# Kernel optimization log

Hardware: AMD Instinct MI355X
Metric: run time of the kernel (lower is better)

Reference implementation:

```python
import jax, jax.numpy as jnp
from jax import lax
import numpy as np

MB, QLEN, EMB, QVS, VOCAB, ANS = 64, 20, 32, 128, 80, 10
CH, D, NOBJ, OBJF, G = 24, 8, 64, 26, 256


def _coord_tensor():
    c = np.zeros((NOBJ, 2), dtype=np.float32)
    for i in range(NOBJ):
        c[i] = [(i // 8 - 2) / 2.0, (i % 8 - 2) / 2.0]
    return jnp.asarray(c)


def conv_bn_relu(x, w, b, g, beta):
    y = lax.conv_general_dilated(x, w, (2, 2), [(1, 1), (1, 1)],
                                 dimension_numbers=("NCHW", "OIHW", "NCHW"))
    y = y + b[None, :, None, None]
    m = y.mean((0, 2, 3), keepdims=True)
    v = y.var((0, 2, 3), keepdims=True)  # biased var, training-mode BN
    y = (y - m) / jnp.sqrt(v + 1e-5) * g[None, :, None, None] + beta[None, :, None, None]
    return jax.nn.relu(y)


def lstm_last(xseq, wih, whh, bih, bhh):
    # xseq: [T, mb, E]; PyTorch gate order i,f,g,o
    H = whh.shape[1]
    h0 = jnp.zeros((xseq.shape[1], H), xseq.dtype)

    def step(carry, x_t):
        h, c = carry
        gates = x_t @ wih.T + bih + h @ whh.T + bhh
        i, f, g, o = jnp.split(gates, 4, axis=-1)
        c = jax.nn.sigmoid(f) * c + jax.nn.sigmoid(i) * jnp.tanh(g)
        h = jax.nn.sigmoid(o) * jnp.tanh(c)
        return (h, c), None

    (h, _), _ = lax.scan(step, (h0, h0), xseq)
    return h


def setup_inputs() -> dict:
    key = jax.random.key(0)
    ks = iter(jax.random.split(key, 64))
    nrm = lambda shape, s=0.05: jax.random.normal(next(ks), shape, jnp.float32) * s
    d = {}
    d["image"] = jax.random.normal(next(ks), (MB, 3, 128, 128), jnp.float32)
    d["question"] = jax.random.randint(next(ks), (MB, QLEN), 0, VOCAB, jnp.int32)
    emb = nrm((VOCAB, EMB), 1.0)
    d["emb"] = emb.at[0].set(0.0)  # padding_idx=0
    d["lstm_wih"] = nrm((4 * QVS, EMB))
    d["lstm_whh"] = nrm((4 * QVS, QVS))
    d["lstm_bih"] = nrm((4 * QVS,))
    d["lstm_bhh"] = nrm((4 * QVS,))
    cin = 3
    for l in range(1, 5):
        d[f"c{l}_w"] = nrm((CH, cin, 3, 3))
        d[f"c{l}_b"] = nrm((CH,))
        d[f"bn{l}_g"] = jnp.ones((CH,), jnp.float32)
        d[f"bn{l}_b"] = jnp.zeros((CH,), jnp.float32)
        cin = CH
    d["g1_w"] = nrm((G, 2 * OBJF + QVS))
    d["g1_b"] = nrm((G,))
    for l in (2, 3, 4):
        d[f"g{l}_w"] = nrm((G, G))
        d[f"g{l}_b"] = nrm((G,))
    d["f1_w"] = nrm((G, G)); d["f1_b"] = nrm((G,))
    d["f2_w"] = nrm((G, G)); d["f2_b"] = nrm((G,))
    d["f3_w"] = nrm((ANS, G)); d["f3_b"] = nrm((ANS,))
    return d


def reference(image, question, emb, lstm_wih, lstm_whh, lstm_bih, lstm_bhh,
              c1_w, c1_b, bn1_g, bn1_b, c2_w, c2_b, bn2_g, bn2_b,
              c3_w, c3_b, bn3_g, bn3_b, c4_w, c4_b, bn4_g, bn4_b,
              g1_w, g1_b, g2_w, g2_b, g3_w, g3_b, g4_w, g4_b,
              f1_w, f1_b, f2_w, f2_b, f3_w, f3_b):
    # question -> LSTM final hidden state
    q = emb[question]                      # [mb, T, E]
    q = jnp.transpose(q, (1, 0, 2))        # [T, mb, E]
    qvec = lstm_last(q, lstm_wih, lstm_whh, lstm_bih, lstm_bhh)  # [mb, QVS]

    # conv tower: 128 -> 64 -> 32 -> 16 -> 8
    x = conv_bn_relu(image, c1_w, c1_b, bn1_g, bn1_b)
    x = conv_bn_relu(x, c2_w, c2_b, bn2_g, bn2_b)
    x = conv_bn_relu(x, c3_w, c3_b, bn3_g, bn3_b)
    x = conv_bn_relu(x, c4_w, c4_b, bn4_g, bn4_b)  # [mb, 24, 8, 8]

    # objects = flattened grid cells + coords -> [mb, 64, 26]
    x_flat = x.reshape(MB, CH, NOBJ).transpose(0, 2, 1)
    coords = jnp.broadcast_to(_coord_tensor()[None], (MB, NOBJ, 2))
    objs = jnp.concatenate([x_flat, coords], axis=-1)

    # g_theta fc1 decomposed over the concat [obj_c(26), obj_r(26), q(128)]
    # so the 180-wide pairwise tensor is never materialized.
    w_i, w_j, w_q = g1_w[:, :OBJF], g1_w[:, OBJF:2 * OBJF], g1_w[:, 2 * OBJF:]
    pre_i = objs @ w_i.T                   # contribution of x_i (column object)
    pre_j = objs @ w_j.T                   # contribution of x_j (row object)
    pre_q = qvec @ w_q.T + g1_b            # [mb, 256]
    h = jax.nn.relu(pre_j[:, :, None, :] + pre_i[:, None, :, :]
                    + pre_q[:, None, None, :])      # [mb, 64, 64, 256]
    h = jax.nn.relu(h @ g2_w.T + g2_b)
    h = jax.nn.relu(h @ g3_w.T + g3_b)
    h = jax.nn.relu(h @ g4_w.T + g4_b)
    x_g = h.sum((1, 2))                    # sum over all 4096 pairs -> [mb, 256]

    # f_phi (dropout as identity / eval mode)
    x_f = jax.nn.relu(x_g @ f1_w.T + f1_b)
    x_f = jax.nn.relu(x_f @ f2_w.T + f2_b)
    x_f = x_f @ f3_w.T + f3_b
    return jax.nn.log_softmax(x_f, axis=-1)
```

## Files before the change

kernel.cpp:

```cpp
#include <hip/hip_runtime.h>
#include <math.h>

#define MBS   64
#define QLENS 20
#define EMBS  32
#define QVSS  128
#define ANSS  10
#define CHS   24
#define NOBJS 64
#define GS    256

typedef __attribute__((ext_vector_type(8))) short short8;
typedef __attribute__((ext_vector_type(4))) float f32x4;
typedef __attribute__((ext_vector_type(16))) float f32x16;

__device__ __forceinline__ unsigned short f2bf(float f) {
  unsigned u = __float_as_uint(f);
  u += 0x7fffu + ((u >> 16) & 1u);
  return (unsigned short)(u >> 16);
}
__device__ __forceinline__ float sigm(float x) { return 1.0f / (1.0f + expf(-x)); }

__global__ __launch_bounds__(256) void prep_k(const float* __restrict__ g2w,
                                              const float* __restrict__ g3w,
                                              const float* __restrict__ g4w,
                                              unsigned short* __restrict__ wbf,
                                              const float* __restrict__ g1w,
                                              float* __restrict__ g1wT,
                                              float* __restrict__ stats) {
  int bidx = blockIdx.x;
  if (bidx == 0) stats[threadIdx.x] = 0.0f;
  if (bidx < 768) {
    int idx = bidx * 256 + threadIdx.x;
    int l = idx >> 16, r = idx & 65535;
    int kt = r >> 12;
    int rem = r & 4095;
    int kh = rem >> 11;
    int n = (rem >> 3) & 255;
    int e = rem & 7;
    const float* src = (l == 0) ? g2w : ((l == 1) ? g3w : g4w);
    wbf[idx] = f2bf(src[n * 256 + kt * 16 + kh * 8 + e]);
  } else {
    int idx = (bidx - 768) * 256 + threadIdx.x;
    int f = idx >> 8, n = idx & 255;
    g1wT[f * 256 + n] = g1w[n * 180 + f];
  }
}

__global__ __launch_bounds__(512) void lstm_k(const int* __restrict__ question,
                                              const float* __restrict__ emb,
                                              const float* __restrict__ wih,
                                              const float* __restrict__ bih,
                                              const float* __restrict__ bhh,
                                              const float* __restrict__ whh,
                                              float* __restrict__ qvec) {
  int b = blockIdx.x;
  int gt = threadIdx.x;
  __shared__ float h[QVSS];
  __shared__ float gates[4 * QVSS];
  __shared__ int toks[QLENS];
  float w[QVSS];
#pragma unroll
  for (int k = 0; k < QVSS; ++k) w[k] = whh[gt * QVSS + k];
  float wi[EMBS];
#pragma unroll
  for (int k = 0; k < EMBS; ++k) wi[k] = wih[gt * EMBS + k];
  float bb = bih[gt] + bhh[gt];
  if (gt < QLENS) toks[gt] = question[b * QLENS + gt];
  float c = 0.0f;
  if (gt < QVSS) h[gt] = 0.0f;
  __syncthreads();
  float xp[QLENS];
#pragma unroll
  for (int t = 0; t < QLENS; ++t) {
    const float* e = emb + toks[t] * EMBS;
    float a = bb;
#pragma unroll
    for (int k = 0; k < EMBS; ++k) a += wi[k] * e[k];
    xp[t] = a;
  }
  for (int t = 0; t < QLENS; ++t) {
    float acc = xp[t];
#pragma unroll
    for (int k4 = 0; k4 < QVSS / 4; ++k4) {
      float4 hv = *reinterpret_cast<const float4*>(&h[k4 * 4]);
      acc += w[k4 * 4 + 0] * hv.x + w[k4 * 4 + 1] * hv.y
           + w[k4 * 4 + 2] * hv.z + w[k4 * 4 + 3] * hv.w;
    }
    gates[gt] = acc;
    __syncthreads();
    if (gt < QVSS) {
      float ig = gates[gt];
      float fg = gates[QVSS + gt];
      float gg = gates[2 * QVSS + gt];
      float og = gates[3 * QVSS + gt];
      c = sigm(fg) * c + sigm(ig) * tanhf(gg);
      h[gt] = sigm(og) * tanhf(c);
    }
    __syncthreads();
  }
  if (gt < QVSS) qvec[b * QVSS + gt] = h[gt];
}

template <int CIN, int H, bool BN>
__global__ __launch_bounds__(256) void conv_k(const float* __restrict__ x,
                                              const float* __restrict__ w,
                                              const float* __restrict__ bias,
                                              float* __restrict__ y,
                                              const float* __restrict__ st,
                                              const float* __restrict__ g,
                                              const float* __restrict__ beta,
                                              float inv_cnt) {
  const int OH = H / 2, GW = OH / 4, CP = CHS / 2;
  __shared__ float4 swp[CHS * CIN * 3];
  __shared__ float sb[CHS];
  __shared__ float ss[CIN], stt[CIN];
  for (int i = threadIdx.x; i < CHS * CIN * 3; i += 256) {
    int kh = i % 3, ci = (i / 3) % CIN, co = i / (3 * CIN);
    const float* wp = w + (co * CIN + ci) * 9 + kh * 3;
    swp[i] = make_float4(wp[0], wp[1], wp[2], 0.0f);
  }
  if (threadIdx.x < CHS) sb[threadIdx.x] = bias[threadIdx.x];
  if (BN && threadIdx.x < CIN) {
    int ci = threadIdx.x;
    float m = st[ci * 2 + 0] * inv_cnt;
    float v = st[ci * 2 + 1] * inv_cnt - m * m;
    float r = rsqrtf(v + 1e-5f);
    ss[ci] = r * g[ci];
    stt[ci] = beta[ci] - m * r * g[ci];
  }
  __syncthreads();
  int idx = blockIdx.x * 256 + threadIdx.x;
  int gg = idx % GW;
  int oh = (idx / GW) % OH;
  int cp = (idx / (GW * OH)) % CP;
  int b  = idx / (CP * OH * GW);
  int co0 = cp * 2, co1 = co0 + 1;
  float a00 = sb[co0], a01 = a00, a02 = a00, a03 = a00;
  float a10 = sb[co1], a11 = a10, a12 = a10, a13 = a10;
  const float* xb = x + b * CIN * H * H;
  const float4* w0 = swp + co0 * CIN * 3;
  const float4* w1 = swp + co1 * CIN * 3;
  bool left = (gg > 0);
#pragma unroll
  for (int kh = 0; kh < 3; ++kh) {
    int ih = oh * 2 - 1 + kh;
    if (ih < 0 || ih >= H) continue;
    for (int ci = 0; ci < CIN; ++ci) {
      const float* row = xb + (ci * H + ih) * H + 8 * gg;
      float4 v1 = *(const float4*)(row);
      float4 v2 = *(const float4*)(row + 4);
      float am1 = left ? row[-1] : 0.0f;
      if (BN) {
        float s = ss[ci], t = stt[ci];
        v1.x = fmaxf(fmaf(v1.x, s, t), 0.0f);
        v1.y = fmaxf(fmaf(v1.y, s, t), 0.0f);
        v1.z = fmaxf(fmaf(v1.z, s, t), 0.0f);
        v1.w = fmaxf(fmaf(v1.w, s, t), 0.0f);
        v2.x = fmaxf(fmaf(v2.x, s, t), 0.0f);
        v2.y = fmaxf(fmaf(v2.y, s, t), 0.0f);
        v2.z = fmaxf(fmaf(v2.z, s, t), 0.0f);
        v2.w = fmaxf(fmaf(v2.w, s, t), 0.0f);
        am1 = left ? fmaxf(fmaf(am1, s, t), 0.0f) : 0.0f;
      }
      float4 wa = w0[ci * 3 + kh];
      float4 wb = w1[ci * 3 + kh];
      a00 = fmaf(wa.x, am1,  a00); a00 = fmaf(wa.y, v1.x, a00); a00 = fmaf(wa.z, v1.y, a00);
      a01 = fmaf(wa.x, v1.y, a01); a01 = fmaf(wa.y, v1.z, a01); a01 = fmaf(wa.z, v1.w, a01);
      a02 = fmaf(wa.x, v1.w, a02); a02 = fmaf(wa.y, v2.x, a02); a02 = fmaf(wa.z, v2.y, a02);
      a03 = fmaf(wa.x, v2.y, a03); a03 = fmaf(wa.y, v2.z, a03); a03 = fmaf(wa.z, v2.w, a03);
      a10 = fmaf(wb.x, am1,  a10); a10 = fmaf(wb.y, v1.x, a10); a10 = fmaf(wb.z, v1.y, a10);
      a11 = fmaf(wb.x, v1.y, a11); a11 = fmaf(wb.y, v1.z, a11); a11 = fmaf(wb.z, v1.w, a11);
      a12 = fmaf(wb.x, v1.w, a12); a12 = fmaf(wb.y, v2.x, a12); a12 = fmaf(wb.z, v2.y, a12);
      a13 = fmaf(wb.x, v2.y, a13); a13 = fmaf(wb.y, v2.z, a13); a13 = fmaf(wb.z, v2.w, a13);
    }
  }
  *(float4*)(y + ((b * CHS + co0) * OH + oh) * OH + 4 * gg) = make_float4(a00, a01, a02, a03);
  *(float4*)(y + ((b * CHS + co1) * OH + oh) * OH + 4 * gg) = make_float4(a10, a11, a12, a13);
}

__global__ __launch_bounds__(256) void stats_k(const float* __restrict__ y,
                                               float* __restrict__ st,
                                               int HW, int SUB) {
  int c = blockIdx.x / SUB, sub = blockIdx.x % SUB;
  int bpb = MBS / SUB;
  float s = 0.0f, s2 = 0.0f;
  for (int b = sub * bpb; b < (sub + 1) * bpb; ++b) {
    const float* p = y + (b * CHS + c) * HW;
    for (int i = threadIdx.x * 4; i < HW; i += 1024) {
      float4 v = *reinterpret_cast<const float4*>(p + i);
      s  += v.x + v.y + v.z + v.w;
      s2 += v.x * v.x + v.y * v.y + v.z * v.z + v.w * v.w;
    }
  }
#pragma unroll
  for (int off = 1; off < 64; off <<= 1) {
    s  += __shfl_xor(s, off);
    s2 += __shfl_xor(s2, off);
  }
  __shared__ float rs[4], rs2[4];
  int w = threadIdx.x >> 6;
  if ((threadIdx.x & 63) == 0) { rs[w] = s; rs2[w] = s2; }
  __syncthreads();
  if (threadIdx.x == 0) {
    atomicAdd(&st[c * 2 + 0], rs[0] + rs[1] + rs[2] + rs[3]);
    atomicAdd(&st[c * 2 + 1], rs2[0] + rs2[1] + rs2[2] + rs2[3]);
  }
}

__global__ __launch_bounds__(256) void pre_k(const float* __restrict__ x4raw,
                                             const float* __restrict__ st,
                                             const float* __restrict__ g,
                                             const float* __restrict__ beta,
                                             const float* __restrict__ g1wT,
                                             const float* __restrict__ g1b,
                                             const float* __restrict__ qvec,
                                             float* __restrict__ pre_i,
                                             float* __restrict__ pre_j,
                                             float* __restrict__ pre_q) {
  int bo = blockIdx.x;
  int n = threadIdx.x;
  __shared__ float sm[QVSS];
  if (bo < 4096) {
    int b = bo >> 6, o = bo & 63;
    if (n < CHS) {
      float m = st[n * 2 + 0] * (1.0f / 4096.0f);
      float v = st[n * 2 + 1] * (1.0f / 4096.0f) - m * m;
      float xv = x4raw[(b * CHS + n) * NOBJS + o];
      sm[n] = fmaxf((xv - m) * rsqrtf(v + 1e-5f) * g[n] + beta[n], 0.0f);
    }
    if (n == 24) sm[24] = (float)(o / 8 - 2) * 0.5f;
    if (n == 25) sm[25] = (float)(o % 8 - 2) * 0.5f;
    __syncthreads();
    float ai = 0.0f, aj = 0.0f;
#pragma unroll
    for (int f = 0; f < 26; ++f) {
      ai += g1wT[f * 256 + n] * sm[f];
      aj += g1wT[(26 + f) * 256 + n] * sm[f];
    }
    pre_i[bo * GS + n] = ai;
    pre_j[bo * GS + n] = aj;
  } else {
    int b = bo - 4096;
    if (n < QVSS) sm[n] = qvec[b * QVSS + n];
    __syncthreads();
    float a = g1b[n];
#pragma unroll
    for (int k = 0; k < QVSS; ++k) a += g1wT[(52 + k) * 256 + n] * sm[k];
    pre_q[b * GS + n] = a;
  }
}

__global__ __launch_bounds__(512, 4) void rel_k(const float* __restrict__ pre_i,
                                                const float* __restrict__ pre_j,
                                                const float* __restrict__ pre_q,
                                                const unsigned short* __restrict__ wbf,
                                                const float* __restrict__ g2b,
                                                const float* __restrict__ g3b,
                                                const float* __restrict__ g4b,
                                                float* __restrict__ xpart) {
  __shared__ short8 hb8[2048];
  char* hb = (char*)hb8;
  int bid = blockIdx.x;
  int b = bid >> 6, j = bid & 63;
  int tid = threadIdx.x;
  int w = tid >> 6, lane = tid & 63;
  int l31 = lane & 31, lh = lane >> 5;

  const short8* Wt = (const short8*)wbf;
  const int nA = w * 32 + l31;
  const int pOff = lh * 256 + nA;

  short8 pa[4];
#pragma unroll
  for (int i = 0; i < 4; ++i) pa[i] = Wt[i * 512 + pOff];

  {
    int r = tid & 63, kc = tid >> 6;
    const float* pj = pre_j + (b * 64 + j) * GS;
    const float* pi = pre_i + (b * 64 + r) * GS;
    const float* pq = pre_q + b * GS;
    int rowbase = r * 512;
    int sw = (r & 31) << 4;
#pragma unroll
    for (int kk = 0; kk < 4; ++kk) {
      int n0 = kc * 32 + kk * 8;
      float4 va  = *(const float4*)(pi + n0);
      float4 va2 = *(const float4*)(pi + n0 + 4);
      float4 vj  = *(const float4*)(pj + n0);
      float4 vj2 = *(const float4*)(pj + n0 + 4);
      float4 vq  = *(const float4*)(pq + n0);
      float4 vq2 = *(const float4*)(pq + n0 + 4);
      short8 pack;
      pack[0] = (short)f2bf(fmaxf(va.x  + vj.x  + vq.x,  0.0f));
      pack[1] = (short)f2bf(fmaxf(va.y  + vj.y  + vq.y,  0.0f));
      pack[2] = (short)f2bf(fmaxf(va.z  + vj.z  + vq.z,  0.0f));
      pack[3] = (short)f2bf(fmaxf(va.w  + vj.w  + vq.w,  0.0f));
      pack[4] = (short)f2bf(fmaxf(va2.x + vj2.x + vq2.x, 0.0f));
      pack[5] = (short)f2bf(fmaxf(va2.y + vj2.y + vq2.y, 0.0f));
      pack[6] = (short)f2bf(fmaxf(va2.z + vj2.z + vq2.z, 0.0f));
      pack[7] = (short)f2bf(fmaxf(va2.w + vj2.w + vq2.w, 0.0f));
      *(short8*)(hb + rowbase + ((n0 * 2) ^ sw)) = pack;
    }
  }
  asm volatile("s_waitcnt lgkmcnt(0)" ::: "memory");
  __builtin_amdgcn_s_barrier();
  __builtin_amdgcn_sched_barrier(0);

  const int rA0 = l31 * 512;
  const int rA1 = (32 + l31) * 512;
  const int swA = l31 << 4;

#pragma unroll 1
  for (int L = 0; L < 3; ++L) {
    const float* bias = (L == 0) ? g2b : ((L == 1) ? g3b : g4b);
    float biasA = bias[nA];
    f32x16 acc0 = {}, acc1 = {};
    short8 a0[2], a1[2];
#pragma unroll
    for (int i = 0; i < 2; ++i) {
      int colb = (i * 32 + lh * 16) ^ swA;
      a0[i] = *(const short8*)(hb + rA0 + colb);
      a1[i] = *(const short8*)(hb + rA1 + colb);
    }
#pragma unroll
    for (int kt = 0; kt < 16; ++kt) {
      short8 nb = Wt[(L * 16 + kt + 4) * 512 + pOff];
      acc0 = __builtin_amdgcn_mfma_f32_32x32x16_bf16(a0[kt & 1], pa[kt & 3], acc0, 0, 0, 0);
      acc1 = __builtin_amdgcn_mfma_f32_32x32x16_bf16(a1[kt & 1], pa[kt & 3], acc1, 0, 0, 0);
      int ktn = (kt < 14) ? kt + 2 : 15;
      int colb = (ktn * 32 + lh * 16) ^ swA;
      a0[kt & 1] = *(const short8*)(hb + rA0 + colb);
      a1[kt & 1] = *(const short8*)(hb + rA1 + colb);
      pa[kt & 3] = nb;
    }
    asm volatile("s_waitcnt lgkmcnt(0)" ::: "memory");
    __builtin_amdgcn_s_barrier();
    __builtin_amdgcn_sched_barrier(0);
    if (L < 2) {
#pragma unroll
      for (int reg = 0; reg < 16; ++reg) {
        int rr = (reg & 3) + 8 * (reg >> 2) + 4 * lh;
        int swr = rr << 4;
        unsigned short v0 = f2bf(fmaxf(acc0[reg] + biasA, 0.0f));
        unsigned short v1 = f2bf(fmaxf(acc1[reg] + biasA, 0.0f));
        *(unsigned short*)(hb + rr * 512        + ((nA * 2) ^ swr)) = v0;
        *(unsigned short*)(hb + (32 + rr) * 512 + ((nA * 2) ^ swr)) = v1;
      }
      asm volatile("s_waitcnt lgkmcnt(0)" ::: "memory");
      __builtin_amdgcn_s_barrier();
      __builtin_amdgcn_sched_barrier(0);
    } else {
      float sA = 0.0f;
#pragma unroll
      for (int reg = 0; reg < 16; ++reg)
        sA += fmaxf(acc0[reg] + biasA, 0.0f) + fmaxf(acc1[reg] + biasA, 0.0f);
      sA += __shfl_xor(sA, 32);
      float* fs = (float*)hb;
      if (lh == 0) fs[nA] = sA;
      asm volatile("s_waitcnt lgkmcnt(0)" ::: "memory");
      __builtin_amdgcn_s_barrier();
      __builtin_amdgcn_sched_barrier(0);
      if (tid < GS) xpart[bid * GS + tid] = fs[tid];
    }
  }
}

__global__ __launch_bounds__(256) void final_k(const float* __restrict__ xpart,
                                               const float* __restrict__ f1w,
                                               const float* __restrict__ f1b,
                                               const float* __restrict__ f2w,
                                               const float* __restrict__ f2b,
                                               const float* __restrict__ f3w,
                                               const float* __restrict__ f3b,
                                               float* __restrict__ out) {
  int b = blockIdx.x, n = threadIdx.x;
  __shared__ float s0[GS], s1[GS], sl[16];
  float xs = 0.0f;
  for (int j = 0; j < 64; ++j) xs += xpart[(b * 64 + j) * GS + n];
  s0[n] = xs;
  __syncthreads();
  float a = f1b[n];
  {
    const float4* wr = (const float4*)(f1w + n * GS);
    for (int k = 0; k < GS / 4; ++k) {
      float4 wv = wr[k];
      a += wv.x * s0[k * 4] + wv.y * s0[k * 4 + 1] + wv.z * s0[k * 4 + 2] + wv.w * s0[k * 4 + 3];
    }
  }
  s1[n] = fmaxf(a, 0.0f);
  __syncthreads();
  a = f2b[n];
  {
    const float4* wr = (const float4*)(f2w + n * GS);
    for (int k = 0; k < GS / 4; ++k) {
      float4 wv = wr[k];
      a += wv.x * s1[k * 4] + wv.y * s1[k * 4 + 1] + wv.z * s1[k * 4 + 2] + wv.w * s1[k * 4 + 3];
    }
  }
  s0[n] = fmaxf(a, 0.0f);
  __syncthreads();
  if (n < ANSS) {
    a = f3b[n];
    const float4* wr = (const float4*)(f3w + n * GS);
    for (int k = 0; k < GS / 4; ++k) {
      float4 wv = wr[k];
      a += wv.x * s0[k * 4] + wv.y * s0[k * 4 + 1] + wv.z * s0[k * 4 + 2] + wv.w * s0[k * 4 + 3];
    }
    sl[n] = a;
  }
  __syncthreads();
  if (n == 0) {
    float m = -1e30f;
    for (int i = 0; i < ANSS; ++i) m = fmaxf(m, sl[i]);
    float s = 0.0f;
    for (int i = 0; i < ANSS; ++i) s += expf(sl[i] - m);
    sl[12] = m + logf(s);
  }
  __syncthreads();
  if (n < ANSS) out[b * ANSS + n] = sl[n] - sl[12];
}

extern "C" void kernel_launch(void* const* d_in, const int* in_sizes, int n_in,
                              void* d_out, int out_size, void* d_ws, size_t ws_size,
                              hipStream_t stream) {
  const float* image = (const float*)d_in[0];
  const int*   question = (const int*)d_in[1];
  const float* emb = (const float*)d_in[2];
  const float* wih = (const float*)d_in[3];
  const float* whh = (const float*)d_in[4];
  const float* bih = (const float*)d_in[5];
  const float* bhh = (const float*)d_in[6];
  const float* c1w = (const float*)d_in[7];
  const float* c1b = (const float*)d_in[8];
  const float* bn1g = (const float*)d_in[9];
  const float* bn1b = (const float*)d_in[10];
  const float* c2w = (const float*)d_in[11];
  const float* c2b = (const float*)d_in[12];
  const float* bn2g = (const float*)d_in[13];
  const float* bn2b = (const float*)d_in[14];
  const float* c3w = (const float*)d_in[15];
  const float* c3b = (const float*)d_in[16];
  const float* bn3g = (const float*)d_in[17];
  const float* bn3b = (const float*)d_in[18];
  const float* c4w = (const float*)d_in[19];
  const float* c4b = (const float*)d_in[20];
  const float* bn4g = (const float*)d_in[21];
  const float* bn4b = (const float*)d_in[22];
  const float* g1w = (const float*)d_in[23];
  const float* g1b = (const float*)d_in[24];
  const float* g2w = (const float*)d_in[25];
  const float* g2b = (const float*)d_in[26];
  const float* g3w = (const float*)d_in[27];
  const float* g3b = (const float*)d_in[28];
  const float* g4w = (const float*)d_in[29];
  const float* g4b = (const float*)d_in[30];
  const float* f1w = (const float*)d_in[31];
  const float* f1b = (const float*)d_in[32];
  const float* f2w = (const float*)d_in[33];
  const float* f2b = (const float*)d_in[34];
  const float* f3w = (const float*)d_in[35];
  const float* f3b = (const float*)d_in[36];
  float* out = (float*)d_out;

  float* wsf = (float*)d_ws;
  float* arenaA = wsf;
  float* arenaB = wsf + 6291456;
  float* qvec   = wsf + 8519680;
  float* pre_i  = wsf + 8527872;
  float* pre_j  = wsf + 9576448;
  float* pre_q  = wsf + 10625024;
  float* stats  = wsf + 10657792;
  unsigned short* wbf = (unsigned short*)(wsf + 10658048);
  float* g1wT   = wsf + 10764544;
  float* xpart  = arenaA;

  prep_k<<<948, 256, 0, stream>>>(g2w, g3w, g4w, wbf, g1w, g1wT, stats);
  lstm_k<<<64, 512, 0, stream>>>(question, emb, wih, bih, bhh, whh, qvec);

  conv_k<3, 128, false><<<3072, 256, 0, stream>>>(image, c1w, c1b, arenaA,
                                                  nullptr, nullptr, nullptr, 0.0f);
  stats_k<<<24 * 16, 256, 0, stream>>>(arenaA, stats + 0, 4096, 16);

  conv_k<24, 64, true><<<768, 256, 0, stream>>>(arenaA, c2w, c2b, arenaB,
                                                stats + 0, bn1g, bn1b, 1.0f / 262144.0f);
  stats_k<<<24 * 16, 256, 0, stream>>>(arenaB, stats + 48, 1024, 16);

  conv_k<24, 32, true><<<192, 256, 0, stream>>>(arenaB, c3w, c3b, arenaA,
                                                stats + 48, bn2g, bn2b, 1.0f / 65536.0f);
  stats_k<<<24 * 4, 256, 0, stream>>>(arenaA, stats + 96, 256, 4);

  conv_k<24, 16, true><<<48, 256, 0, stream>>>(arenaA, c4w, c4b, arenaB,
                                               stats + 96, bn3g, bn3b, 1.0f / 16384.0f);
  stats_k<<<24, 256, 0, stream>>>(arenaB, stats + 144, 64, 1);

  pre_k<<<4096 + 64, 256, 0, stream>>>(arenaB, stats + 144, bn4g, bn4b, g1wT, g1b, qvec,
                                       pre_i, pre_j, pre_q);

  rel_k<<<4096, 512, 0, stream>>>(pre_i, pre_j, pre_q, wbf, g2b, g3b, g4b, xpart);

  final_k<<<64, 256, 0, stream>>>(xpart, f1w, f1b, f2w, f2b, f3w, f3b, out);
}
```

Baseline: 379.6 us.

## Fuse BatchNorm statistics into conv epilogue with bucketed atomics

Removes the separate stats_k reduction kernels and accumulates per-channel sum and sum-of-squares directly in each conv kernel's epilogue, using wave shuffles and block reduction. Atomics go into 16 buckets to spread contention, and consumers sum the buckets when computing mean and variance. This saves four launches and a full re-read of each conv output, at the cost of more atomics, a larger stats buffer zeroed by the prep kernel, and shifted workspace offsets.

```diff
diff --git a/kernel.cpp b/kernel.cpp
--- a/kernel.cpp
+++ b/kernel.cpp
@@ -9,6 +9,7 @@
 #define CHS   24
 #define NOBJS 64
 #define GS    256
+#define NBKT  16
 
 typedef __attribute__((ext_vector_type(8))) short short8;
 typedef __attribute__((ext_vector_type(4))) float f32x4;
@@ -29,7 +30,7 @@
                                               float* __restrict__ g1wT,
                                               float* __restrict__ stats) {
   int bidx = blockIdx.x;
-  if (bidx == 0) stats[threadIdx.x] = 0.0f;
+  if (bidx < 12) stats[bidx * 256 + threadIdx.x] = 0.0f;
   if (bidx < 768) {
     int idx = bidx * 256 + threadIdx.x;
     int l = idx >> 16, r = idx & 65535;
@@ -107,14 +108,18 @@
                                               const float* __restrict__ w,
                                               const float* __restrict__ bias,
                                               float* __restrict__ y,
-                                              const float* __restrict__ st,
+                                              const float* __restrict__ st_in,
                                               const float* __restrict__ g,
                                               const float* __restrict__ beta,
-                                              float inv_cnt) {
+                                              float inv_cnt,
+                                              float* __restrict__ st_out) {
   const int OH = H / 2, GW = OH / 4, CP = CHS / 2;
+  constexpr int TPC0 = (H / 2) * (H / 8);
+  constexpr int TPC = (TPC0 >= 256) ? 256 : TPC0;
   __shared__ float4 swp[CHS * CIN * 3];
   __shared__ float sb[CHS];
   __shared__ float ss[CIN], stt[CIN];
+  __shared__ float red[4][4];
   for (int i = threadIdx.x; i < CHS * CIN * 3; i += 256) {
     int kh = i % 3, ci = (i / 3) % CIN, co = i / (3 * CIN);
     const float* wp = w + (co * CIN + ci) * 9 + kh * 3;
@@ -123,8 +128,13 @@
   if (threadIdx.x < CHS) sb[threadIdx.x] = bias[threadIdx.x];
   if (BN && threadIdx.x < CIN) {
     int ci = threadIdx.x;
-    float m = st[ci * 2 + 0] * inv_cnt;
-    float v = st[ci * 2 + 1] * inv_cnt - m * m;
+    float s = 0.0f, s2 = 0.0f;
+    for (int bkt = 0; bkt < NBKT; ++bkt) {
+      s  += st_in[(bkt * CHS + ci) * 2 + 0];
+      s2 += st_in[(bkt * CHS + ci) * 2 + 1];
+    }
+    float m = s * inv_cnt;
+    float v = s2 * inv_cnt - m * m;
     float r = rsqrtf(v + 1e-5f);
     ss[ci] = r * g[ci];
     stt[ci] = beta[ci] - m * r * g[ci];
@@ -177,34 +187,37 @@
   }
   *(float4*)(y + ((b * CHS + co0) * OH + oh) * OH + 4 * gg) = make_float4(a00, a01, a02, a03);
   *(float4*)(y + ((b * CHS + co1) * OH + oh) * OH + 4 * gg) = make_float4(a10, a11, a12, a13);
-}
-
-__global__ __launch_bounds__(256) void stats_k(const float* __restrict__ y,
-                                               float* __restrict__ st,
-                                               int HW, int SUB) {
-  int c = blockIdx.x / SUB, sub = blockIdx.x % SUB;
-  int bpb = MBS / SUB;
-  float s = 0.0f, s2 = 0.0f;
-  for (int b = sub * bpb; b < (sub + 1) * bpb; ++b) {
-    const float* p = y + (b * CHS + c) * HW;
-    for (int i = threadIdx.x * 4; i < HW; i += 1024) {
-      float4 v = *reinterpret_cast<const float4*>(p + i);
-      s  += v.x + v.y + v.z + v.w;
-      s2 += v.x * v.x + v.y * v.y + v.z * v.z + v.w * v.w;
-    }
-  }
-#pragma unroll
-  for (int off = 1; off < 64; off <<= 1) {
-    s  += __shfl_xor(s, off);
-    s2 += __shfl_xor(s2, off);
-  }
-  __shared__ float rs[4], rs2[4];
-  int w = threadIdx.x >> 6;
-  if ((threadIdx.x & 63) == 0) { rs[w] = s; rs2[w] = s2; }
-  __syncthreads();
-  if (threadIdx.x == 0) {
-    atomicAdd(&st[c * 2 + 0], rs[0] + rs[1] + rs[2] + rs[3]);
-    atomicAdd(&st[c * 2 + 1], rs2[0] + rs2[1] + rs2[2] + rs2[3]);
+
+  float s0 = a00 + a01 + a02 + a03;
+  float q0 = a00 * a00 + a01 * a01 + a02 * a02 + a03 * a03;
+  float s1 = a10 + a11 + a12 + a13;
+  float q1 = a10 * a10 + a11 * a11 + a12 * a12 + a13 * a13;
+  constexpr int WR = (TPC < 64) ? TPC : 64;
+#pragma unroll
+  for (int off = 1; off < WR; off <<= 1) {
+    s0 += __shfl_xor(s0, off); q0 += __shfl_xor(q0, off);
+    s1 += __shfl_xor(s1, off); q1 += __shfl_xor(q1, off);
+  }
+  int bkt = blockIdx.x & (NBKT - 1);
+  if (TPC == 256) {
+    int wv = threadIdx.x >> 6;
+    if ((threadIdx.x & 63) == 0) {
+      red[wv][0] = s0; red[wv][1] = q0; red[wv][2] = s1; red[wv][3] = q1;
+    }
+    __syncthreads();
+    if (threadIdx.x == 0) {
+      atomicAdd(&st_out[(bkt * CHS + co0) * 2 + 0], red[0][0] + red[1][0] + red[2][0] + red[3][0]);
+      atomicAdd(&st_out[(bkt * CHS + co0) * 2 + 1], red[0][1] + red[1][1] + red[2][1] + red[3][1]);
+      atomicAdd(&st_out[(bkt * CHS + co1) * 2 + 0], red[0][2] + red[1][2] + red[2][2] + red[3][2]);
+      atomicAdd(&st_out[(bkt * CHS + co1) * 2 + 1], red[0][3] + red[1][3] + red[2][3] + red[3][3]);
+    }
+  } else {
+    if ((threadIdx.x & (TPC - 1)) == 0) {
+      atomicAdd(&st_out[(bkt * CHS + co0) * 2 + 0], s0);
+      atomicAdd(&st_out[(bkt * CHS + co0) * 2 + 1], q0);
+      atomicAdd(&st_out[(bkt * CHS + co1) * 2 + 0], s1);
+      atomicAdd(&st_out[(bkt * CHS + co1) * 2 + 1], q1);
+    }
   }
 }
 
@@ -224,8 +237,13 @@
   if (bo < 4096) {
     int b = bo >> 6, o = bo & 63;
     if (n < CHS) {
-      float m = st[n * 2 + 0] * (1.0f / 4096.0f);
-      float v = st[n * 2 + 1] * (1.0f / 4096.0f) - m * m;
+      float s = 0.0f, s2 = 0.0f;
+      for (int bkt = 0; bkt < NBKT; ++bkt) {
+        s  += st[(bkt * CHS + n) * 2 + 0];
+        s2 += st[(bkt * CHS + n) * 2 + 1];
+      }
+      float m = s * (1.0f / 4096.0f);
+      float v = s2 * (1.0f / 4096.0f) - m * m;
       float xv = x4raw[(b * CHS + n) * NOBJS + o];
       sm[n] = fmaxf((xv - m) * rsqrtf(v + 1e-5f) * g[n] + beta[n], 0.0f);
     }
@@ -471,30 +489,27 @@
   float* pre_j  = wsf + 9576448;
   float* pre_q  = wsf + 10625024;
   float* stats  = wsf + 10657792;
-  unsigned short* wbf = (unsigned short*)(wsf + 10658048);
-  float* g1wT   = wsf + 10764544;
+  unsigned short* wbf = (unsigned short*)(wsf + 10660864);
+  float* g1wT   = wsf + 10767360;
   float* xpart  = arenaA;
 
   prep_k<<<948, 256, 0, stream>>>(g2w, g3w, g4w, wbf, g1w, g1wT, stats);
   lstm_k<<<64, 512, 0, stream>>>(question, emb, wih, bih, bhh, whh, qvec);
 
   conv_k<3, 128, false><<<3072, 256, 0, stream>>>(image, c1w, c1b, arenaA,
-                                                  nullptr, nullptr, nullptr, 0.0f);
-  stats_k<<<24 * 16, 256, 0, stream>>>(arenaA, stats + 0, 4096, 16);
-
+                                                  nullptr, nullptr, nullptr, 0.0f,
+                                                  stats + 0);
   conv_k<24, 64, true><<<768, 256, 0, stream>>>(arenaA, c2w, c2b, arenaB,
-                                                stats + 0, bn1g, bn1b, 1.0f / 262144.0f);
-  stats_k<<<24 * 16, 256, 0, stream>>>(arenaB, stats + 48, 1024, 16);
-
+                                                stats + 0, bn1g, bn1b, 1.0f / 262144.0f,
+                                                stats + 768);
   conv_k<24, 32, true><<<192, 256, 0, stream>>>(arenaB, c3w, c3b, arenaA,
-                                                stats + 48, bn2g, bn2b, 1.0f / 65536.0f);
-  stats_k<<<24 * 4, 256, 0, stream>>>(arenaA, stats + 96, 256, 4);
-
+                                                stats + 768, bn2g, bn2b, 1.0f / 65536.0f,
+                                                stats + 1536);
   conv_k<24, 16, true><<<48, 256, 0, stream>>>(arenaA, c4w, c4b, arenaB,
-                                               stats + 96, bn3g, bn3b, 1.0f / 16384.0f);
-  stats_k<<<24, 256, 0, stream>>>(arenaB, stats + 144, 64, 1);
-
-  pre_k<<<4096 + 64, 256, 0, stream>>>(arenaB, stats + 144, bn4g, bn4b, g1wT, g1b, qvec,
+                                               stats + 1536, bn3g, bn3b, 1.0f / 16384.0f,
+                                               stats + 2304);
+
+  pre_k<<<4096 + 64, 256, 0, stream>>>(arenaB, stats + 2304, bn4g, bn4b, g1wT, g1b, qvec,
                                        pre_i, pre_j, pre_q);
 
   rel_k<<<4096, 512, 0, stream>>>(pre_i, pre_j, pre_q, wbf, g2b, g3b, g4b, xpart);
```

Result: faster. 338.3 us (-10.9%).
